# Kernel optimization log

Measured on AMD Instinct MI355X. Metric: run time of the kernel, lower is better.

The kernel has to match this reference:

```python
import jax, jax.numpy as jnp
import numpy as np

TAU = 0.96      # init_tau
N_OUT = 48      # readout neurons (last n_out of the merged population)
V_TH = 1.0      # LIF firing threshold

@jax.custom_vjp
def spike_fn(v):
    # Heaviside firing with triangle surrogate gradient
    return (v >= V_TH).astype(v.dtype)

def _spike_fwd(v):
    return spike_fn(v), v

def _spike_bwd(v, g):
    # TriangleCall surrogate: grad = max(0, 1 - |v - v_th|)
    return (g * jnp.maximum(0.0, 1.0 - jnp.abs(v - V_TH)),)

spike_fn.defvjp(_spike_fwd, _spike_bwd)


def setup_inputs() -> dict:
    key = jax.random.key(0)
    k1, k2, k3, k4 = jax.random.split(key, 4)
    B, T, n_in = 256, 100, 512
    n_hidden, n_out = 2000, 48
    N = n_hidden + n_out  # 2048
    x = jax.random.uniform(k1, (B, T, n_in), dtype=jnp.float32)
    # nn.Linear default init U(-1/sqrt(fan_in), 1/sqrt(fan_in)), scaled by 3, frozen
    bound = 1.0 / np.sqrt(n_in)
    W_fc = 3.0 * jax.random.uniform(k2, (N, n_in), minval=-bound, maxval=bound, dtype=jnp.float32)
    recurrent = jax.random.uniform(k3, (N, N), dtype=jnp.float32) / np.sqrt(N)
    mask = jnp.ones((N, N), jnp.float32) - jnp.eye(N, dtype=jnp.float32)  # no self-connections
    binary = (jax.random.uniform(k4, (N, N)) > 0.3).astype(jnp.float32)
    return {"x": x, "W_fc": W_fc, "recurrent": recurrent, "mask": mask, "binary": binary}


def reference(x, W_fc, recurrent, mask, binary):
    B = x.shape[0]
    N = recurrent.shape[0]
    eff_rec = recurrent * mask * binary                    # [N, N]
    # feed-forward currents for all timesteps at once: [B, T, N]
    cur_in = jnp.einsum('btn,mn->btm', x, W_fc)

    def step(carry, c_t):
        mem, spike = carry                                 # each [B, N]
        cur = c_t + spike @ eff_rec                        # recurrent drive
        mem = TAU * mem * (1.0 - spike) + cur              # LIF decay + hard reset
        spike = spike_fn(mem)
        return (mem, spike), spike[:, -N_OUT:]

    init = (jnp.zeros((B, N), x.dtype), jnp.zeros((B, N), x.dtype))
    _, outs = jax.lax.scan(step, init, jnp.swapaxes(cur_in, 0, 1))  # [T, B, n_out]
    return jnp.swapaxes(outs, 0, 1)                        # [B, T, n_out]
```

## Files before the change

### kernel.cpp

```cpp
#include <hip/hip_runtime.h>

typedef unsigned short u16;
typedef signed char s8;
typedef __attribute__((ext_vector_type(8))) short short8;
typedef __attribute__((ext_vector_type(4))) float f32x4;
typedef __attribute__((ext_vector_type(4))) unsigned short u16x4;
typedef __attribute__((ext_vector_type(4))) int i32x4;
typedef __attribute__((ext_vector_type(4))) unsigned int u32x4;

#define TT 100
#define NB 256
#define NN 2048
#define KREC 4096
#define NPRE 2
#define EPS 0.25f
#define WMAXC 0.1325826f
#define INV_SW (127.0f / WMAXC)
#define S_DEQ (WMAXC / 16129.0f)

#define OFF_WH    0ull
#define OFF_WL    2097152ull
#define OFF_WQ    4194304ull
#define OFF_XH4   5242880ull
#define OFF_XL4   6291456ull
#define OFF_XQ    7340032ull
#define OFF_BC    20447232ull
#define OFF_COLS  37224448ull
#define OFF_PARTC 37232640ull
#define OFF_FFPRE 37494784ull
#define OFF_SPK   45883392ull
#define OFF_MEMB  46931968ull
#define OFF_PART  49029120ull
#define OFF_FLAGS 65806336ull
#define OFF_AF    65806400ull
#define OFF_SYNC  65806912ull

__device__ __forceinline__ u16 f2bf(float f){
    unsigned int x = __float_as_uint(f);
    x += 0x7fffu + ((x >> 16) & 1u);
    return (u16)(x >> 16);
}
__device__ __forceinline__ float bf2f(u16 u){
    return __uint_as_float(((unsigned int)u) << 16);
}

__global__ void prep_all(const float* __restrict__ x, const float* __restrict__ Wfc,
                         u16* __restrict__ Wh, u16* __restrict__ Wl, s8* __restrict__ Wq,
                         u16* __restrict__ xh4, u16* __restrict__ xl4, s8* __restrict__ xq)
{
    int bid = blockIdx.x;
    if (bid < 6400){
        int idx = bid * 256 + threadIdx.x;
        int b = idx / (TT * 64);
        int r = idx - b * (TT * 64);
        int t = r >> 6;
        int c = r & 63;
        const float* gx = x + ((size_t)b * TT + t) * 512 + (c << 3);
        f32x4 f0 = *reinterpret_cast<const f32x4*>(gx);
        f32x4 f1 = *reinterpret_cast<const f32x4*>(gx + 4);
        unsigned long long q = 0;
        #pragma unroll
        for (int i = 0; i < 4; ++i)
            q |= (unsigned long long)(unsigned)__float2int_rn(f0[i] * 127.0f) << (8 * i);
        #pragma unroll
        for (int i = 0; i < 4; ++i)
            q |= (unsigned long long)(unsigned)__float2int_rn(f1[i] * 127.0f) << (8 * (i + 4));
        size_t o = ((size_t)t * NB + b) * 512 + (c << 3);
        *reinterpret_cast<unsigned long long*>(xq + o) = q;
        if (t < 4){
            short8 vh, vl;
            #pragma unroll
            for (int i = 0; i < 4; ++i){
                u16 h0 = f2bf(f0[i]);
                vh[i] = (short)h0; vl[i] = (short)f2bf(f0[i] - bf2f(h0));
                u16 h1 = f2bf(f1[i]);
                vh[i + 4] = (short)h1; vl[i + 4] = (short)f2bf(f1[i] - bf2f(h1));
            }
            *reinterpret_cast<short8*>(xh4 + o) = vh;
            *reinterpret_cast<short8*>(xl4 + o) = vl;
        }
    } else {
        int idx = (bid - 6400) * 256 + threadIdx.x;
        float v = Wfc[idx];
        u16 h = f2bf(v);
        Wh[idx] = h;
        Wl[idx] = f2bf(v - bf2f(h));
        Wq[idx] = (s8)__float2int_rn(v * INV_SW);
    }
}

__global__ void prep_rec(const float* __restrict__ rec, const float* __restrict__ msk,
                         const float* __restrict__ bin, u16* __restrict__ Bc,
                         float* __restrict__ partc){
    __shared__ u16 hs[64][66];
    __shared__ u16 ls[64][66];
    __shared__ float redc[4][64];
    int tid = threadIdx.x;
    int tm = tid & 63, t4 = tid >> 6;
    int m0 = blockIdx.x * 64, n0 = blockIdx.y * 64;
    float accl = 0.f;
    #pragma unroll
    for (int j = 0; j < 16; ++j){
        int nl = t4 + j * 4;
        size_t gi = (size_t)(n0 + nl) * NN + m0 + tm;
        float e = rec[gi] * msk[gi] * bin[gi];
        u16 h = f2bf(e);
        hs[nl][tm] = h;
        ls[nl][tm] = f2bf(e - bf2f(h));
        accl += e;
    }
    redc[t4][tm] = accl;
    __syncthreads();
    if (t4 == 0)
        partc[(size_t)blockIdx.y * NN + m0 + tm] =
            redc[0][tm] + redc[1][tm] + redc[2][tm] + redc[3][tm];
    #pragma unroll
    for (int j = 0; j < 16; ++j){
        int ml = t4 + j * 4;
        size_t o = (size_t)(m0 + ml) * KREC + n0 + tm;
        Bc[o]        = hs[tm][ml];
        Bc[o + 2048] = ls[tm][ml];
    }
}

__global__ __launch_bounds__(512, 2) void fused_gemm(const s8* __restrict__ xq,
    const s8* __restrict__ Wq, const u16* __restrict__ xh4, const u16* __restrict__ xl4,
    const u16* __restrict__ Wh, const u16* __restrict__ Wl,
    const float* __restrict__ partc, float* __restrict__ cs, float* __restrict__ ffpre,
    int* __restrict__ AF, float* __restrict__ out)
{
    __shared__ u16 Ab[2][8192];
    __shared__ u16 Bb[2][8192];
    __shared__ float csL[256];
    __shared__ int redH[8];
    const int tid = threadIdx.x, lane = tid & 63, w = tid >> 6;
    const int l7 = lane & 7, l8 = lane >> 3;
    const int bid = blockIdx.x;

    if (bid >= 96){
        const int bid2 = bid - 96;
        const int logical = (bid2 & 7) * 200 + (bid2 >> 3);
        const int mt = logical >> 3;
        const int bn = logical & 7;
        const int wm = w >> 2, wn = w & 3;

        if (tid < 256){
            float s = 0.f;
            #pragma unroll
            for (int c = 0; c < 32; ++c) s += partc[(size_t)c * NN + bn * 256 + tid];
            csL[tid] = s;
        }

        char* As_ = reinterpret_cast<char*>(Ab);
        char* Bs_ = reinterpret_cast<char*>(Bb);
        const int row_s = tid >> 2, gr = tid & 3;
        const int swA = ((row_s << 6) | (gr << 4)) ^ ((row_s & 7) << 4);
        const s8* gA = xq + (size_t)(mt * 128 + row_s) * 512 + gr * 16;
        int swB[2];
        const s8* gBp[2];
        #pragma unroll
        for (int j = 0; j < 2; ++j){
            int rb = j * 128 + row_s;
            swB[j] = ((rb << 6) | (gr << 4)) ^ ((rb & 7) << 4);
            gBp[j] = Wq + (size_t)(bn * 256 + rb) * 512 + gr * 16;
        }

        *reinterpret_cast<u32x4*>(As_ + swA) = *reinterpret_cast<const u32x4*>(gA);
        #pragma unroll
        for (int j = 0; j < 2; ++j)
            *reinterpret_cast<u32x4*>(Bs_ + swB[j]) = *reinterpret_cast<const u32x4*>(gBp[j]);
        __syncthreads();

        i32x4 acc[4][4];
        #pragma unroll
        for (int mi = 0; mi < 4; ++mi)
            #pragma unroll
            for (int ni = 0; ni < 4; ++ni) acc[mi][ni] = (i32x4){0, 0, 0, 0};

        u32x4 na, nb0, nb1;
        const int kgb = (lane >> 4) << 4;
        for (int kt = 0; kt < 8; ++kt){
            int sel = kt & 1;
            if (kt + 1 < 8){
                na  = *reinterpret_cast<const u32x4*>(gA + (kt + 1) * 64);
                nb0 = *reinterpret_cast<const u32x4*>(gBp[0] + (kt + 1) * 64);
                nb1 = *reinterpret_cast<const u32x4*>(gBp[1] + (kt + 1) * 64);
            }
            const char* ab = As_ + sel * 8192;
            const char* bb3 = Bs_ + sel * 16384;
            i32x4 afr[4];
            #pragma unroll
            for (int mi = 0; mi < 4; ++mi){
                int r = wm * 64 + mi * 16 + (lane & 15);
                int off = ((r << 6) | kgb) ^ ((r & 7) << 4);
                afr[mi] = *reinterpret_cast<const i32x4*>(ab + off);
            }
            #pragma unroll
            for (int ni = 0; ni < 4; ++ni){
                int r = wn * 64 + ni * 16 + (lane & 15);
                int off = ((r << 6) | kgb) ^ ((r & 7) << 4);
                i32x4 bfr = *reinterpret_cast<const i32x4*>(bb3 + off);
                #pragma unroll
                for (int mi = 0; mi < 4; ++mi)
                    acc[mi][ni] = __builtin_amdgcn_mfma_i32_16x16x64_i8(afr[mi], bfr, acc[mi][ni], 0, 0, 0);
            }
            if (kt + 1 < 8){
                int osel = (kt + 1) & 1;
                *reinterpret_cast<u32x4*>(As_ + osel * 8192 + swA) = na;
                *reinterpret_cast<u32x4*>(Bs_ + osel * 16384 + swB[0]) = nb0;
                *reinterpret_cast<u32x4*>(Bs_ + osel * 16384 + swB[1]) = nb1;
            }
            __syncthreads();
        }

        const int r4 = (lane >> 4) << 2;
        const int cfrag = lane & 15;
        const int t_out = mt >> 1;
        int ok = 1;
        #pragma unroll
        for (int mi = 0; mi < 4; ++mi)
            #pragma unroll
            for (int ni = 0; ni < 4; ++ni){
                int nl = wn * 64 + ni * 16 + cfrag;
                int n = bn * 256 + nl;
                float csv = csL[nl];
                #pragma unroll
                for (int jj = 0; jj < 4; ++jj){
                    int m = mt * 128 + wm * 64 + mi * 16 + r4 + jj;
                    float v = (float)acc[mi][ni][jj] * S_DEQ + csv;
                    ok &= (v >= 1.0f + EPS) ? 1 : 0;
                    if (bn == 7 && n >= 2000){
                        int b = m & 255;
                        out[((size_t)b * TT + t_out) * 48 + (n - 2000)] = (v >= 1.0f) ? 1.f : 0.f;
                    }
                }
            }
        unsigned long long bb = __ballot(ok != 0);
        if (lane == 0) redH[w] = (bb == ~0ull) ? 1 : 0;
        __syncthreads();
        if (tid == 0){
            int a = 1;
            #pragma unroll
            for (int i = 0; i < 8; ++i) a &= redH[i];
            atomicAnd(&AF[t_out], a ? ~0 : 0);
        }
    } else {
        const int bn = bid & 15;
        const int mt = bid >> 4;
        const int wm = w >> 2, wn = w & 3;

        if (mt == 0 && tid < 128){
            float s = 0.f;
            #pragma unroll
            for (int c = 0; c < 32; ++c) s += partc[(size_t)c * NN + bn * 128 + tid];
            cs[bn * 128 + tid] = s;
        }

        auto load_tile = [&](int kt, short8* pa, short8* pb){
            int reg = kt >> 3;
            int kk = (kt & 7) * 64;
            const u16* ab = (reg == 2) ? xl4 : xh4;
            const u16* bb2 = (reg == 1) ? Wl : Wh;
            #pragma unroll
            for (int j = 0; j < 2; ++j){
                int chunk = w * 2 + j;
                int row = chunk * 8 + l8;
                pa[j] = *reinterpret_cast<const short8*>(ab + (size_t)(mt * 128 + row) * 512 + kk + (l7 << 3));
                pb[j] = *reinterpret_cast<const short8*>(bb2 + (size_t)(bn * 128 + row) * 512 + kk + (l7 << 3));
            }
        };
        auto write_tile = [&](int sel, const short8* pa, const short8* pb){
            #pragma unroll
            for (int j = 0; j < 2; ++j){
                int chunk = w * 2 + j;
                int idx = chunk * 512 + l8 * 64 + ((l7 ^ l8) << 3);
                *reinterpret_cast<short8*>(&Ab[sel][idx]) = pa[j];
                *reinterpret_cast<short8*>(&Bb[sel][idx]) = pb[j];
            }
        };

        f32x4 zero = {0.f, 0.f, 0.f, 0.f};
        f32x4 acc[4][2];
        #pragma unroll
        for (int mi = 0; mi < 4; ++mi)
            #pragma unroll
            for (int ni = 0; ni < 2; ++ni) acc[mi][ni] = zero;

        short8 ra[2], rb[2], na[2], nb[2];
        load_tile(0, ra, rb);
        write_tile(0, ra, rb);
        __syncthreads();

        for (int kt = 0; kt < 24; ++kt){
            int sel = kt & 1;
            if (kt + 1 < 24) load_tile(kt + 1, na, nb);
            #pragma unroll
            for (int kk2 = 0; kk2 < 2; ++kk2){
                int ke = kk2 * 32 + ((lane >> 4) << 3);
                short8 af[4], bfr[2];
                #pragma unroll
                for (int mi = 0; mi < 4; ++mi){
                    int row = wm * 64 + mi * 16 + (lane & 15);
                    int byte = (row * 128 + ke * 2) ^ ((row & 7) << 4);
                    af[mi] = *reinterpret_cast<const short8*>(reinterpret_cast<const char*>(Ab[sel]) + byte);
                }
                #pragma unroll
                for (int ni = 0; ni < 2; ++ni){
                    int row = wn * 32 + ni * 16 + (lane & 15);
                    int byte = (row * 128 + ke * 2) ^ ((row & 7) << 4);
                    bfr[ni] = *reinterpret_cast<const short8*>(reinterpret_cast<const char*>(Bb[sel]) + byte);
                }
                #pragma unroll
                for (int mi = 0; mi < 4; ++mi)
                    #pragma unroll
                    for (int ni = 0; ni < 2; ++ni)
                        acc[mi][ni] = __builtin_amdgcn_mfma_f32_16x16x32_bf16(af[mi], bfr[ni], acc[mi][ni], 0, 0, 0);
            }
            if (kt + 1 < 24) write_tile((kt + 1) & 1, na, nb);
            __syncthreads();
        }

        const int r4 = (lane >> 4) << 2;
        const int c  = lane & 15;
        #pragma unroll
        for (int mi = 0; mi < 4; ++mi)
            #pragma unroll
            for (int ni = 0; ni < 2; ++ni){
                int n = bn * 128 + wn * 32 + ni * 16 + c;
                #pragma unroll
                for (int jj = 0; jj < 4; ++jj){
                    int m = mt * 128 + wm * 64 + mi * 16 + r4 + jj;
                    ffpre[(size_t)m * NN + n] = acc[mi][ni][jj];
                }
            }
    }
}


__device__ __forceinline__ void lif_finish(int b, int n0, const float mem[4], int t,
    u16* __restrict__ spk, float* __restrict__ memb, float* __restrict__ out,
    int* __restrict__ flags, int* red, int tid, int lane, int w)
{
    int s[4];
    u16x4 sv; f32x4 mv;
    #pragma unroll
    for (int k = 0; k < 4; ++k){
        s[k] = (mem[k] >= 1.0f) ? 1 : 0;
        sv[k] = s[k] ? (u16)0x3F80 : (u16)0;
        mv[k] = mem[k];
    }
    *reinterpret_cast<u16x4*>(spk + (size_t)b * NN + n0) = sv;
    *reinterpret_cast<f32x4*>(memb + (size_t)b * NN + n0) = mv;
    if (n0 >= 2000){
        #pragma unroll
        for (int k = 0; k < 4; ++k)
            out[((size_t)b * TT + t) * 48 + (n0 + k - 2000)] = s[k] ? 1.f : 0.f;
    }
    int af = s[0] & s[1] & s[2] & s[3];
    int az = !(s[0] | s[1] | s[2] | s[3]);
    unsigned long long ba = __ballot(af != 0);
    unsigned long long bz = __ballot(az != 0);
    if (lane == 0) red[w] = ((ba == ~0ull) ? 1 : 0) | ((bz == ~0ull) ? 2 : 0);
    __syncthreads();
    if (tid == 0){
        int a = 3;
        #pragma unroll
        for (int i = 0; i < 8; ++i) a &= red[i];
        atomicAnd(&flags[t], 0xFFFFFFFC | a);
    }
}

__global__ __launch_bounds__(512) void lif0(const float* __restrict__ ffpre,
    u16* __restrict__ spk, float* __restrict__ memb, float* __restrict__ out,
    int* __restrict__ flags)
{
    __shared__ int red[8];
    const int tid = threadIdx.x, lane = tid & 63, w = tid >> 6;
    const int b = blockIdx.x, n0 = tid << 2;
    f32x4 fe = *reinterpret_cast<const f32x4*>(ffpre + (size_t)b * NN + n0);
    float m[4];
    #pragma unroll
    for (int k = 0; k < 4; ++k) m[k] = fe[k];
    lif_finish(b, n0, m, 0, spk, memb, out, flags, red, tid, lane, w);
}

__global__ __launch_bounds__(512, 2) void gemm_pre(
    const u16* __restrict__ Bc, const u16* __restrict__ spk,
    const int* __restrict__ flags, float* __restrict__ part, int t)
{
    if (flags[t - 1] & 3) return;
    __shared__ u16 Ab[2][8192];
    __shared__ u16 Bb[2][8192];
    const int tid = threadIdx.x, lane = tid & 63, w = tid >> 6;
    const int l7 = lane & 7, l8 = lane >> 3;
    const int bid = blockIdx.x;
    const int bn = bid & 15, my = (bid >> 4) & 1, ks = bid >> 5;
    const int kstart = ks << 9, acol = kstart & 2047;
    const int wm = w >> 2, wn = w & 3;

    auto load_tile = [&](int kt, short8* pa, short8* pb){
        int k0 = kt * 64;
        #pragma unroll
        for (int j = 0; j < 2; ++j){
            int chunk = w * 2 + j;
            int row = chunk * 8 + l8;
            const u16* ga = spk + (size_t)(my * 128 + row) * NN + acol + k0 + (l7 << 3);
            pa[j] = *reinterpret_cast<const short8*>(ga);
            const u16* gb = Bc + (size_t)(bn * 128 + row) * KREC + kstart + k0 + (l7 << 3);
            pb[j] = *reinterpret_cast<const short8*>(gb);
        }
    };
    auto write_tile = [&](int sel, const short8* pa, const short8* pb){
        #pragma unroll
        for (int j = 0; j < 2; ++j){
            int chunk = w * 2 + j;
            int idx = chunk * 512 + l8 * 64 + ((l7 ^ l8) << 3);
            *reinterpret_cast<short8*>(&Ab[sel][idx]) = pa[j];
            *reinterpret_cast<short8*>(&Bb[sel][idx]) = pb[j];
        }
    };

    f32x4 zero = {0.f, 0.f, 0.f, 0.f};
    f32x4 acc[4][2];
    #pragma unroll
    for (int mi = 0; mi < 4; ++mi)
        #pragma unroll
        for (int ni = 0; ni < 2; ++ni) acc[mi][ni] = zero;

    short8 ra[2], rb[2], na[2], nb[2];
    load_tile(0, ra, rb);
    write_tile(0, ra, rb);
    __syncthreads();

    for (int kt = 0; kt < 8; ++kt){
        int sel = kt & 1;
        if (kt + 1 < 8) load_tile(kt + 1, na, nb);
        #pragma unroll
        for (int kk2 = 0; kk2 < 2; ++kk2){
            int ke = kk2 * 32 + ((lane >> 4) << 3);
            short8 af2[4], bfr[2];
            #pragma unroll
            for (int mi = 0; mi < 4; ++mi){
                int row = wm * 64 + mi * 16 + (lane & 15);
                int byte = (row * 128 + ke * 2) ^ ((row & 7) << 4);
                af2[mi] = *reinterpret_cast<const short8*>(reinterpret_cast<const char*>(Ab[sel]) + byte);
            }
            #pragma unroll
            for (int ni = 0; ni < 2; ++ni){
                int row = wn * 32 + ni * 16 + (lane & 15);
                int byte = (row * 128 + ke * 2) ^ ((row & 7) << 4);
                bfr[ni] = *reinterpret_cast<const short8*>(reinterpret_cast<const char*>(Bb[sel]) + byte);
            }
            #pragma unroll
            for (int mi = 0; mi < 4; ++mi)
                #pragma unroll
                for (int ni = 0; ni < 2; ++ni)
                    acc[mi][ni] = __builtin_amdgcn_mfma_f32_16x16x32_bf16(af2[mi], bfr[ni], acc[mi][ni], 0, 0, 0);
        }
        if (kt + 1 < 8) write_tile((kt + 1) & 1, na, nb);
        __syncthreads();
    }

    float* pp = part + (size_t)ks * (NB * NN);
    const int r4 = (lane >> 4) << 2;
    const int c  = lane & 15;
    #pragma unroll
    for (int mi = 0; mi < 4; ++mi)
        #pragma unroll
        for (int ni = 0; ni < 2; ++ni){
            int n = bn * 128 + wn * 32 + ni * 16 + c;
            #pragma unroll
            for (int jj = 0; jj < 4; ++jj){
                int b = my * 128 + wm * 64 + mi * 16 + r4 + jj;
                pp[(size_t)b * NN + n] = acc[mi][ni][jj];
            }
        }
}

__global__ __launch_bounds__(512) void lif_pre(const float* __restrict__ ffpre,
    const float* __restrict__ colsum, const float* __restrict__ part,
    const int* __restrict__ AF, u16* __restrict__ spk, float* __restrict__ memb,
    float* __restrict__ out, int* __restrict__ flags, int t)
{
    __shared__ int red[8];
    const int tid = threadIdx.x, lane = tid & 63, w = tid >> 6;
    const int b = blockIdx.x, n0 = tid << 2;
    int fl = flags[t - 1] & 3;
    float m[4];

    if (fl & 1){
        if (AF[t] != 0){
            if (b == 0 && tid == 0) flags[t] = 1;
            return;
        }
        f32x4 cs = *reinterpret_cast<const f32x4*>(colsum + n0);
        f32x4 fe = *reinterpret_cast<const f32x4*>(ffpre + ((size_t)t * NB + b) * NN + n0);
        #pragma unroll
        for (int k = 0; k < 4; ++k) m[k] = cs[k] + fe[k];
    } else if (fl & 2){
        f32x4 mb = *reinterpret_cast<const f32x4*>(memb + (size_t)b * NN + n0);
        f32x4 fe = *reinterpret_cast<const f32x4*>(ffpre + ((size_t)t * NB + b) * NN + n0);
        #pragma unroll
        for (int k = 0; k < 4; ++k) m[k] = 0.96f * mb[k] + fe[k];
    } else {
        f32x4 mb = *reinterpret_cast<const f32x4*>(memb + (size_t)b * NN + n0);
        u16x4 sp = *reinterpret_cast<const u16x4*>(spk + (size_t)b * NN + n0);
        f32x4 fe = *reinterpret_cast<const f32x4*>(ffpre + ((size_t)t * NB + b) * NN + n0);
        float p[4] = {0.f, 0.f, 0.f, 0.f};
        #pragma unroll
        for (int ks2 = 0; ks2 < 8; ++ks2){
            f32x4 pv = *reinterpret_cast<const f32x4*>(part + (size_t)ks2 * (NB * NN) + (size_t)b * NN + n0);
            #pragma unroll
            for (int k = 0; k < 4; ++k) p[k] += pv[k];
        }
        #pragma unroll
        for (int k = 0; k < 4; ++k){
            float sprev = sp[k] ? 1.f : 0.f;
            m[k] = 0.96f * mb[k] * (1.f - sprev) + p[k] + fe[k];
        }
    }
    lif_finish(b, n0, m, t, spk, memb, out, flags, red, tid, lane, w);
}

__global__ __launch_bounds__(512, 1) void snn_tail(
    const u16* __restrict__ Bc, const float* __restrict__ x, const float* __restrict__ Wfc,
    const float* __restrict__ colsum, const int* __restrict__ AF, const int* __restrict__ flags,
    u16* __restrict__ spk, float* __restrict__ memb, float* __restrict__ part,
    int* __restrict__ sync, float* __restrict__ out)
{
    __shared__ u16 Ab[2][8192];
    __shared__ u16 Bb[2][8192];
    __shared__ float xrow[512];
    __shared__ int red[8];
    __shared__ int bcast;
    __shared__ int firstbad;
    const int tid = threadIdx.x, lane = tid & 63, w = tid >> 6;
    const int l7 = lane & 7, l8 = lane >> 3;
    const int bid = blockIdx.x;
    int* cnt = sync;
    int* gen = sync + 1;
    int* vote = sync + 2;
    const int b_own = bid;
    const int n0 = tid << 2;
    const int bn = bid & 15, my = (bid >> 4) & 1, ks = bid >> 5;
    const int kstart = ks << 9, acol = kstart & 2047;
    const int wm = w >> 2, wn = w & 3;

    auto gbar = [&](){
        asm volatile("s_waitcnt vmcnt(0) lgkmcnt(0)" ::: "memory");
        __syncthreads();
        if (tid == 0){
            __threadfence();
            int g = __hip_atomic_load(gen, __ATOMIC_RELAXED, __HIP_MEMORY_SCOPE_AGENT);
            int a = __hip_atomic_fetch_add(cnt, 1, __ATOMIC_ACQ_REL, __HIP_MEMORY_SCOPE_AGENT);
            if (a == (int)gridDim.x - 1){
                __hip_atomic_store(cnt, 0, __ATOMIC_RELAXED, __HIP_MEMORY_SCOPE_AGENT);
                __hip_atomic_fetch_add(gen, 1, __ATOMIC_RELEASE, __HIP_MEMORY_SCOPE_AGENT);
            } else {
                while (__hip_atomic_load(gen, __ATOMIC_ACQUIRE, __HIP_MEMORY_SCOPE_AGENT) == g)
                    __builtin_amdgcn_s_sleep(2);
            }
            __threadfence();
        }
        __syncthreads();
    };

    auto wait_vote = [&](int t)->int{
        if (tid == 0){
            int v;
            while (((unsigned)(v = __hip_atomic_load(&vote[t], __ATOMIC_ACQUIRE, __HIP_MEMORY_SCOPE_AGENT)) >> 20) != 256u)
                __builtin_amdgcn_s_sleep(2);
            bcast = v;
        }
        __syncthreads();
        int v = bcast;
        __syncthreads();
        int naf = ((v & 0x3FF) == 256) ? 1 : 0;
        int naz = (((v >> 10) & 0x3FF) == 256) ? 2 : 0;
        return naf | naz;
    };

    auto finish_step = [&](f32x4 m, int t){
        int s[4];
        u16x4 sv;
        #pragma unroll
        for (int k = 0; k < 4; ++k){
            s[k] = (m[k] >= 1.0f) ? 1 : 0;
            sv[k] = s[k] ? (u16)0x3F80 : (u16)0;
        }
        *reinterpret_cast<u16x4*>(spk + (size_t)b_own * NN + n0) = sv;
        *reinterpret_cast<f32x4*>(memb + (size_t)b_own * NN + n0) = m;
        if (n0 >= 2000){
            #pragma unroll
            for (int k = 0; k < 4; ++k)
                out[((size_t)b_own * TT + t) * 48 + (n0 + k - 2000)] = s[k] ? 1.f : 0.f;
        }
        int af = s[0] & s[1] & s[2] & s[3];
        int az = !(s[0] | s[1] | s[2] | s[3]);
        unsigned long long ba = __ballot(af != 0);
        unsigned long long bz = __ballot(az != 0);
        if (lane == 0) red[w] = ((ba == ~0ull) ? 1 : 0) | ((bz == ~0ull) ? 2 : 0);
        __syncthreads();
        if (tid == 0){
            int a = 3;
            #pragma unroll
            for (int i = 0; i < 8; ++i) a &= red[i];
            __hip_atomic_fetch_add(&vote[t], (1 << 20) | (a & 1) | ((a >> 1) << 10),
                                   __ATOMIC_RELEASE, __HIP_MEMORY_SCOPE_AGENT);
        }
        __syncthreads();
    };

    auto load_ff = [&](int tq)->f32x4{
        __syncthreads();
        xrow[tid & 511] = x[((size_t)b_own * TT + tq) * 512 + (tid & 511)];
        __syncthreads();
        f32x4 f = {0.f, 0.f, 0.f, 0.f};
        for (int k = 0; k < 512; ++k){
            float xv = xrow[k];
            #pragma unroll
            for (int j = 0; j < 4; ++j)
                f[j] += xv * Wfc[(size_t)(n0 + j) * 512 + k];
        }
        return f;
    };

    int pv = flags[NPRE] & 3;
    int t = NPRE + 1;

    while (t < TT){
        if (pv & 1){
            if (tid == 0) firstbad = TT;
            __syncthreads();
            int idx = t + tid;
            if (idx < TT && AF[idx] == 0) atomicMin(&firstbad, idx);
            __syncthreads();
            int h = firstbad;
            if (h == TT) return;
            f32x4 cs = *reinterpret_cast<const f32x4*>(colsum + n0);
            f32x4 ffv = load_ff(h);
            f32x4 m;
            #pragma unroll
            for (int k = 0; k < 4; ++k) m[k] = cs[k] + ffv[k];
            finish_step(m, h);
            pv = wait_vote(h);
            t = h + 1;
        } else if (pv & 2){
            f32x4 ffv = load_ff(t);
            f32x4 mb = *reinterpret_cast<const f32x4*>(memb + (size_t)b_own * NN + n0);
            f32x4 m;
            #pragma unroll
            for (int k = 0; k < 4; ++k) m[k] = 0.96f * mb[k] + ffv[k];
            finish_step(m, t);
            pv = wait_vote(t);
            ++t;
        } else {
            gbar();
            auto load_tile = [&](int kt, short8* pa, short8* pb){
                int k0 = kt * 64;
                #pragma unroll
                for (int j = 0; j < 2; ++j){
                    int chunk = w * 2 + j;
                    int row = chunk * 8 + l8;
                    const u16* ga = spk + (size_t)(my * 128 + row) * NN + acol + k0 + (l7 << 3);
                    pa[j] = *reinterpret_cast<const short8*>(ga);
                    const u16* gb = Bc + (size_t)(bn * 128 + row) * KREC + kstart + k0 + (l7 << 3);
                    pb[j] = *reinterpret_cast<const short8*>(gb);
                }
            };
            auto write_tile = [&](int sel, const short8* pa, const short8* pb){
                #pragma unroll
                for (int j = 0; j < 2; ++j){
                    int chunk = w * 2 + j;
                    int idx = chunk * 512 + l8 * 64 + ((l7 ^ l8) << 3);
                    *reinterpret_cast<short8*>(&Ab[sel][idx]) = pa[j];
                    *reinterpret_cast<short8*>(&Bb[sel][idx]) = pb[j];
                }
            };

            f32x4 zero = {0.f, 0.f, 0.f, 0.f};
            f32x4 acc[4][2];
            #pragma unroll
            for (int mi = 0; mi < 4; ++mi)
                #pragma unroll
                for (int ni = 0; ni < 2; ++ni) acc[mi][ni] = zero;

            short8 ra[2], rb[2], na[2], nb[2];
            load_tile(0, ra, rb);
            write_tile(0, ra, rb);
            __syncthreads();

            for (int kt = 0; kt < 8; ++kt){
                int sel = kt & 1;
                if (kt + 1 < 8) load_tile(kt + 1, na, nb);
                #pragma unroll
                for (int kk2 = 0; kk2 < 2; ++kk2){
                    int ke = kk2 * 32 + ((lane >> 4) << 3);
                    short8 af2[4], bfr[2];
                    #pragma unroll
                    for (int mi = 0; mi < 4; ++mi){
                        int row = wm * 64 + mi * 16 + (lane & 15);
                        int byte = (row * 128 + ke * 2) ^ ((row & 7) << 4);
                        af2[mi] = *reinterpret_cast<const short8*>(reinterpret_cast<const char*>(Ab[sel]) + byte);
                    }
                    #pragma unroll
                    for (int ni = 0; ni < 2; ++ni){
                        int row = wn * 32 + ni * 16 + (lane & 15);
                        int byte = (row * 128 + ke * 2) ^ ((row & 7) << 4);
                        bfr[ni] = *reinterpret_cast<const short8*>(reinterpret_cast<const char*>(Bb[sel]) + byte);
                    }
                    #pragma unroll
                    for (int mi = 0; mi < 4; ++mi)
                        #pragma unroll
                        for (int ni = 0; ni < 2; ++ni)
                            acc[mi][ni] = __builtin_amdgcn_mfma_f32_16x16x32_bf16(af2[mi], bfr[ni], acc[mi][ni], 0, 0, 0);
                }
                if (kt + 1 < 8) write_tile((kt + 1) & 1, na, nb);
                __syncthreads();
            }

            float* pp = part + (size_t)ks * (NB * NN);
            const int r4 = (lane >> 4) << 2;
            const int c  = lane & 15;
            #pragma unroll
            for (int mi = 0; mi < 4; ++mi)
                #pragma unroll
                for (int ni = 0; ni < 2; ++ni){
                    int n = bn * 128 + wn * 32 + ni * 16 + c;
                    #pragma unroll
                    for (int jj = 0; jj < 4; ++jj){
                        int b = my * 128 + wm * 64 + mi * 16 + r4 + jj;
                        pp[(size_t)b * NN + n] = acc[mi][ni][jj];
                    }
                }
            gbar();

            f32x4 ffv = load_ff(t);
            f32x4 mb = *reinterpret_cast<const f32x4*>(memb + (size_t)b_own * NN + n0);
            u16x4 sp = *reinterpret_cast<const u16x4*>(spk + (size_t)b_own * NN + n0);
            float p[4] = {0.f, 0.f, 0.f, 0.f};
            #pragma unroll
            for (int ks2 = 0; ks2 < 8; ++ks2){
                f32x4 pvv = *reinterpret_cast<const f32x4*>(part + (size_t)ks2 * (NB * NN) + (size_t)b_own * NN + n0);
                #pragma unroll
                for (int k = 0; k < 4; ++k) p[k] += pvv[k];
            }
            f32x4 m;
            #pragma unroll
            for (int k = 0; k < 4; ++k){
                float sprev = sp[k] ? 1.f : 0.f;
                m[k] = 0.96f * mb[k] * (1.f - sprev) + p[k] + ffv[k];
            }
            finish_step(m, t);
            pv = wait_vote(t);
            ++t;
        }
    }
}

extern "C" void kernel_launch(void* const* d_in, const int* in_sizes, int n_in,
                              void* d_out, int out_size, void* d_ws, size_t ws_size,
                              hipStream_t stream)
{
    const float* x   = (const float*)d_in[0];
    const float* Wfc = (const float*)d_in[1];
    const float* rec = (const float*)d_in[2];
    const float* msk = (const float*)d_in[3];
    const float* bin = (const float*)d_in[4];
    float* out = (float*)d_out;
    char* ws = (char*)d_ws;

    u16* Wh      = (u16*)(ws + OFF_WH);
    u16* Wl      = (u16*)(ws + OFF_WL);
    s8*  Wq      = (s8*)(ws + OFF_WQ);
    u16* xh4     = (u16*)(ws + OFF_XH4);
    u16* xl4     = (u16*)(ws + OFF_XL4);
    s8*  xq      = (s8*)(ws + OFF_XQ);
    u16* Bc      = (u16*)(ws + OFF_BC);
    float* cs    = (float*)(ws + OFF_COLS);
    float* partc = (float*)(ws + OFF_PARTC);
    float* ffpre = (float*)(ws + OFF_FFPRE);
    u16* spk     = (u16*)(ws + OFF_SPK);
    float* memb  = (float*)(ws + OFF_MEMB);
    float* part  = (float*)(ws + OFF_PART);
    int* flags   = (int*)(ws + OFF_FLAGS);
    int* AF      = (int*)(ws + OFF_AF);
    int* sync    = (int*)(ws + OFF_SYNC);

    hipMemsetAsync(flags, 0xFF, 576, stream);
    hipMemsetAsync(sync, 0, 1024, stream);

    prep_all<<<10496, 256, 0, stream>>>(x, Wfc, Wh, Wl, Wq, xh4, xl4, xq);
    prep_rec<<<dim3(32, 32), 256, 0, stream>>>(rec, msk, bin, Bc, partc);
    fused_gemm<<<1696, 512, 0, stream>>>(xq, Wq, xh4, xl4, Wh, Wl, partc, cs, ffpre, AF, out);
    lif0<<<256, 512, 0, stream>>>(ffpre, spk, memb, out, flags);
    for (int t = 1; t <= NPRE; ++t){
        gemm_pre<<<256, 512, 0, stream>>>(Bc, spk, flags, part, t);
        lif_pre<<<256, 512, 0, stream>>>(ffpre, cs, part, AF, spk, memb, out, flags, t);
    }
    snn_tail<<<256, 512, 0, stream>>>(Bc, x, Wfc, cs, AF, flags, spk, memb, part, sync, out);
}
```

Baseline: 129.9 us.

## Merge prep kernels, retile bf16 GEMM blocks, prefetch int8 tiles two ahead

```diff
diff --git a/kernel.cpp b/kernel.cpp
--- a/kernel.cpp
+++ b/kernel.cpp
@@ -45,9 +45,15 @@
 }
 
 __global__ void prep_all(const float* __restrict__ x, const float* __restrict__ Wfc,
+                         const float* __restrict__ rec, const float* __restrict__ msk,
+                         const float* __restrict__ bin,
                          u16* __restrict__ Wh, u16* __restrict__ Wl, s8* __restrict__ Wq,
-                         u16* __restrict__ xh4, u16* __restrict__ xl4, s8* __restrict__ xq)
+                         u16* __restrict__ xh4, u16* __restrict__ xl4, s8* __restrict__ xq,
+                         u16* __restrict__ Bc, float* __restrict__ partc)
 {
+    __shared__ u16 hs[64][66];
+    __shared__ u16 ls[64][66];
+    __shared__ float redc[4][64];
     int bid = blockIdx.x;
     if (bid < 6400){
         int idx = bid * 256 + threadIdx.x;
@@ -79,47 +85,42 @@
             *reinterpret_cast<short8*>(xh4 + o) = vh;
             *reinterpret_cast<short8*>(xl4 + o) = vl;
         }
-    } else {
+    } else if (bid < 10496){
         int idx = (bid - 6400) * 256 + threadIdx.x;
         float v = Wfc[idx];
         u16 h = f2bf(v);
         Wh[idx] = h;
         Wl[idx] = f2bf(v - bf2f(h));
         Wq[idx] = (s8)__float2int_rn(v * INV_SW);
-    }
-}
-
-__global__ void prep_rec(const float* __restrict__ rec, const float* __restrict__ msk,
-                         const float* __restrict__ bin, u16* __restrict__ Bc,
-                         float* __restrict__ partc){
-    __shared__ u16 hs[64][66];
-    __shared__ u16 ls[64][66];
-    __shared__ float redc[4][64];
-    int tid = threadIdx.x;
-    int tm = tid & 63, t4 = tid >> 6;
-    int m0 = blockIdx.x * 64, n0 = blockIdx.y * 64;
-    float accl = 0.f;
-    #pragma unroll
-    for (int j = 0; j < 16; ++j){
-        int nl = t4 + j * 4;
-        size_t gi = (size_t)(n0 + nl) * NN + m0 + tm;
-        float e = rec[gi] * msk[gi] * bin[gi];
-        u16 h = f2bf(e);
-        hs[nl][tm] = h;
-        ls[nl][tm] = f2bf(e - bf2f(h));
-        accl += e;
-    }
-    redc[t4][tm] = accl;
-    __syncthreads();
-    if (t4 == 0)
-        partc[(size_t)blockIdx.y * NN + m0 + tm] =
-            redc[0][tm] + redc[1][tm] + redc[2][tm] + redc[3][tm];
-    #pragma unroll
-    for (int j = 0; j < 16; ++j){
-        int ml = t4 + j * 4;
-        size_t o = (size_t)(m0 + ml) * KREC + n0 + tm;
-        Bc[o]        = hs[tm][ml];
-        Bc[o + 2048] = ls[tm][ml];
+    } else {
+        int r2 = bid - 10496;
+        int bx = r2 & 31, by = r2 >> 5;
+        int tid = threadIdx.x;
+        int tm = tid & 63, t4 = tid >> 6;
+        int m0 = bx * 64, n0 = by * 64;
+        float accl = 0.f;
+        #pragma unroll
+        for (int j = 0; j < 16; ++j){
+            int nl = t4 + j * 4;
+            size_t gi = (size_t)(n0 + nl) * NN + m0 + tm;
+            float e = rec[gi] * msk[gi] * bin[gi];
+            u16 h = f2bf(e);
+            hs[nl][tm] = h;
+            ls[nl][tm] = f2bf(e - bf2f(h));
+            accl += e;
+        }
+        redc[t4][tm] = accl;
+        __syncthreads();
+        if (t4 == 0)
+            partc[(size_t)by * NN + m0 + tm] =
+                redc[0][tm] + redc[1][tm] + redc[2][tm] + redc[3][tm];
+        #pragma unroll
+        for (int j = 0; j < 16; ++j){
+            int ml = t4 + j * 4;
+            size_t o = (size_t)(m0 + ml) * KREC + n0 + tm;
+            Bc[o]        = hs[tm][ml];
+            Bc[o + 2048] = ls[tm][ml];
+        }
     }
 }
 
@@ -129,7 +130,7 @@
     const float* __restrict__ partc, float* __restrict__ cs, float* __restrict__ ffpre,
     int* __restrict__ AF, float* __restrict__ out)
 {
-    __shared__ u16 Ab[2][8192];
+    __shared__ u16 Ab[2][4096];
     __shared__ u16 Bb[2][8192];
     __shared__ float csL[256];
     __shared__ int redH[8];
@@ -137,8 +138,8 @@
     const int l7 = lane & 7, l8 = lane >> 3;
     const int bid = blockIdx.x;
 
-    if (bid >= 96){
-        const int bid2 = bid - 96;
+    if (bid >= 192){
+        const int bid2 = bid - 192;
         const int logical = (bid2 & 7) * 200 + (bid2 >> 3);
         const int mt = logical >> 3;
         const int bn = logical & 7;
@@ -169,6 +170,9 @@
         #pragma unroll
         for (int j = 0; j < 2; ++j)
             *reinterpret_cast<u32x4*>(Bs_ + swB[j]) = *reinterpret_cast<const u32x4*>(gBp[j]);
+        u32x4 na  = *reinterpret_cast<const u32x4*>(gA + 64);
+        u32x4 nb0 = *reinterpret_cast<const u32x4*>(gBp[0] + 64);
+        u32x4 nb1 = *reinterpret_cast<const u32x4*>(gBp[1] + 64);
         __syncthreads();
 
         i32x4 acc[4][4];
@@ -177,14 +181,20 @@
             #pragma unroll
             for (int ni = 0; ni < 4; ++ni) acc[mi][ni] = (i32x4){0, 0, 0, 0};
 
-        u32x4 na, nb0, nb1;
         const int kgb = (lane >> 4) << 4;
+        #pragma unroll
         for (int kt = 0; kt < 8; ++kt){
-            int sel = kt & 1;
-            if (kt + 1 < 8){
-                na  = *reinterpret_cast<const u32x4*>(gA + (kt + 1) * 64);
-                nb0 = *reinterpret_cast<const u32x4*>(gBp[0] + (kt + 1) * 64);
-                nb1 = *reinterpret_cast<const u32x4*>(gBp[1] + (kt + 1) * 64);
+            const int sel = kt & 1;
+            if (kt < 7){
+                const int os = sel ^ 1;
+                *reinterpret_cast<u32x4*>(As_ + os * 8192 + swA) = na;
+                *reinterpret_cast<u32x4*>(Bs_ + os * 16384 + swB[0]) = nb0;
+                *reinterpret_cast<u32x4*>(Bs_ + os * 16384 + swB[1]) = nb1;
+                if (kt + 2 < 8){
+                    na  = *reinterpret_cast<const u32x4*>(gA + (kt + 2) * 64);
+                    nb0 = *reinterpret_cast<const u32x4*>(gBp[0] + (kt + 2) * 64);
+                    nb1 = *reinterpret_cast<const u32x4*>(gBp[1] + (kt + 2) * 64);
+                }
             }
             const char* ab = As_ + sel * 8192;
             const char* bb3 = Bs_ + sel * 16384;
@@ -203,12 +213,6 @@
                 #pragma unroll
                 for (int mi = 0; mi < 4; ++mi)
                     acc[mi][ni] = __builtin_amdgcn_mfma_i32_16x16x64_i8(afr[mi], bfr, acc[mi][ni], 0, 0, 0);
-            }
-            if (kt + 1 < 8){
-                int osel = (kt + 1) & 1;
-                *reinterpret_cast<u32x4*>(As_ + osel * 8192 + swA) = na;
-                *reinterpret_cast<u32x4*>(Bs_ + osel * 16384 + swB[0]) = nb0;
-                *reinterpret_cast<u32x4*>(Bs_ + osel * 16384 + swB[1]) = nb1;
             }
             __syncthreads();
         }
@@ -261,32 +265,34 @@
             int kk = (kt & 7) * 64;
             const u16* ab = (reg == 2) ? xl4 : xh4;
             const u16* bb2 = (reg == 1) ? Wl : Wh;
+            {
+                int row = w * 8 + l8;
+                pa[0] = *reinterpret_cast<const short8*>(ab + (size_t)(mt * 64 + row) * 512 + kk + (l7 << 3));
+            }
             #pragma unroll
             for (int j = 0; j < 2; ++j){
                 int chunk = w * 2 + j;
                 int row = chunk * 8 + l8;
-                pa[j] = *reinterpret_cast<const short8*>(ab + (size_t)(mt * 128 + row) * 512 + kk + (l7 << 3));
                 pb[j] = *reinterpret_cast<const short8*>(bb2 + (size_t)(bn * 128 + row) * 512 + kk + (l7 << 3));
             }
         };
         auto write_tile = [&](int sel, const short8* pa, const short8* pb){
+            *reinterpret_cast<short8*>(&Ab[sel][w * 512 + l8 * 64 + ((l7 ^ l8) << 3)]) = pa[0];
             #pragma unroll
             for (int j = 0; j < 2; ++j){
                 int chunk = w * 2 + j;
-                int idx = chunk * 512 + l8 * 64 + ((l7 ^ l8) << 3);
-                *reinterpret_cast<short8*>(&Ab[sel][idx]) = pa[j];
-                *reinterpret_cast<short8*>(&Bb[sel][idx]) = pb[j];
+                *reinterpret_cast<short8*>(&Bb[sel][chunk * 512 + l8 * 64 + ((l7 ^ l8) << 3)]) = pb[j];
             }
         };
 
         f32x4 zero = {0.f, 0.f, 0.f, 0.f};
-        f32x4 acc[4][2];
-        #pragma unroll
-        for (int mi = 0; mi < 4; ++mi)
+        f32x4 acc[2][2];
+        #pragma unroll
+        for (int mi = 0; mi < 2; ++mi)
             #pragma unroll
             for (int ni = 0; ni < 2; ++ni) acc[mi][ni] = zero;
 
-        short8 ra[2], rb[2], na[2], nb[2];
+        short8 ra[1], rb[2], na[1], nb[2];
         load_tile(0, ra, rb);
         write_tile(0, ra, rb);
         __syncthreads();
@@ -297,10 +303,10 @@
             #pragma unroll
             for (int kk2 = 0; kk2 < 2; ++kk2){
                 int ke = kk2 * 32 + ((lane >> 4) << 3);
-                short8 af[4], bfr[2];
-                #pragma unroll
-                for (int mi = 0; mi < 4; ++mi){
-                    int row = wm * 64 + mi * 16 + (lane & 15);
+                short8 af[2], bfr[2];
+                #pragma unroll
+                for (int mi = 0; mi < 2; ++mi){
+                    int row = wm * 32 + mi * 16 + (lane & 15);
                     int byte = (row * 128 + ke * 2) ^ ((row & 7) << 4);
                     af[mi] = *reinterpret_cast<const short8*>(reinterpret_cast<const char*>(Ab[sel]) + byte);
                 }
@@ -311,7 +317,7 @@
                     bfr[ni] = *reinterpret_cast<const short8*>(reinterpret_cast<const char*>(Bb[sel]) + byte);
                 }
                 #pragma unroll
-                for (int mi = 0; mi < 4; ++mi)
+                for (int mi = 0; mi < 2; ++mi)
                     #pragma unroll
                     for (int ni = 0; ni < 2; ++ni)
                         acc[mi][ni] = __builtin_amdgcn_mfma_f32_16x16x32_bf16(af[mi], bfr[ni], acc[mi][ni], 0, 0, 0);
@@ -323,13 +329,13 @@
         const int r4 = (lane >> 4) << 2;
         const int c  = lane & 15;
         #pragma unroll
-        for (int mi = 0; mi < 4; ++mi)
+        for (int mi = 0; mi < 2; ++mi)
             #pragma unroll
             for (int ni = 0; ni < 2; ++ni){
                 int n = bn * 128 + wn * 32 + ni * 16 + c;
                 #pragma unroll
                 for (int jj = 0; jj < 4; ++jj){
-                    int m = mt * 128 + wm * 64 + mi * 16 + r4 + jj;
+                    int m = mt * 64 + wm * 32 + mi * 16 + r4 + jj;
                     ffpre[(size_t)m * NN + n] = acc[mi][ni][jj];
                 }
             }
@@ -790,9 +796,8 @@
     hipMemsetAsync(flags, 0xFF, 576, stream);
     hipMemsetAsync(sync, 0, 1024, stream);
 
-    prep_all<<<10496, 256, 0, stream>>>(x, Wfc, Wh, Wl, Wq, xh4, xl4, xq);
-    prep_rec<<<dim3(32, 32), 256, 0, stream>>>(rec, msk, bin, Bc, partc);
-    fused_gemm<<<1696, 512, 0, stream>>>(xq, Wq, xh4, xl4, Wh, Wl, partc, cs, ffpre, AF, out);
+    prep_all<<<11520, 256, 0, stream>>>(x, Wfc, rec, msk, bin, Wh, Wl, Wq, xh4, xl4, xq, Bc, partc);
+    fused_gemm<<<1792, 512, 0, stream>>>(xq, Wq, xh4, xl4, Wh, Wl, partc, cs, ffpre, AF, out);
     lif0<<<256, 512, 0, stream>>>(ffpre, spk, memb, out, flags);
     for (int t = 1; t <= NPRE; ++t){
         gemm_pre<<<256, 512, 0, stream>>>(Bc, spk, flags, part, t);
```

Measured after the change: 129.0 us, median of 2. Within noise of the previous version (-0.7%).
